# Kernel tuning notes

Hardware: AMD Instinct MI355X
Metric: run time of the kernel (lower is better)

## Reference

```python
import jax, jax.numpy as jnp
import numpy as np

B, E, K, U = 2048, 96, 8, 1024  # batch, word_emb_size, num_basis, num_units


def setup_inputs() -> dict:
    key = jax.random.key(0)
    k1, k2, k3, k4, k5 = jax.random.split(key, 5)
    inputs = jax.random.normal(k1, (B, E + K), dtype=jnp.float32)
    h_tm1 = jax.random.normal(k2, (B, U), dtype=jnp.float32)
    c_tm1 = jax.random.normal(k3, (B, U), dtype=jnp.float32)
    basis_kernel = jax.random.normal(k4, (E, K, 4 * U), dtype=jnp.float32) * 0.05
    basis_recurrent_kernel = jax.random.normal(k5, (U, K, 4 * U), dtype=jnp.float32) * 0.05
    bias = jnp.zeros((4 * U,), dtype=jnp.float32)
    return {
        "inputs": inputs,
        "h_tm1": h_tm1,
        "c_tm1": c_tm1,
        "basis_kernel": basis_kernel,
        "basis_recurrent_kernel": basis_recurrent_kernel,
        "bias": bias,
    }


def reference(inputs, h_tm1, c_tm1, basis_kernel, basis_recurrent_kernel, bias):
    word_emb_size = basis_kernel.shape[0]
    num_units = basis_recurrent_kernel.shape[0]
    x = inputs[:, :word_emb_size]           # [B, E]
    c_prob = inputs[:, word_emb_size:]      # [B, K]
    # Algebraically identical to composing a per-example kernel
    # (sum_k c_prob[b,k] * W[:,k,:]) and doing a per-example matmul:
    # z[b,z] = sum_e sum_k x[b,e] * c_prob[b,k] * W[e,k,z] (+ recurrent term).
    z = (jnp.einsum('be,ekz,bk->bz', x, basis_kernel, c_prob)
         + jnp.einsum('bu,ukz,bk->bz', h_tm1, basis_recurrent_kernel, c_prob)
         + bias)
    z0, z1, z2, z3 = jnp.split(z, 4, axis=1)  # each [B, U]
    i = jax.nn.sigmoid(z0)
    f = jax.nn.sigmoid(z1)
    c = f * c_tm1 + i * jnp.tanh(z2)
    o = jax.nn.sigmoid(z3)
    h = o * jnp.tanh(c)
    return (h, c)
```

## Files before the change

kernel.cpp:

```cpp
#include <hip/hip_runtime.h>
#include <stdint.h>
#include <stddef.h>

#define B_SZ   2048
#define E_SZ   96
#define K_SZ   8
#define U_SZ   1024
#define EK     (E_SZ * K_SZ)
#define KD     ((E_SZ + U_SZ) * K_SZ)
#define NZ     (4 * U_SZ)

typedef _Float16 f16_t;
typedef _Float16 f16x8 __attribute__((ext_vector_type(8)));
typedef float    f32x4 __attribute__((ext_vector_type(4)));

typedef __attribute__((address_space(3))) void       lds_void;
typedef const __attribute__((address_space(1))) void gbl_void;

__device__ __forceinline__ void gload16(const void* g, void* l) {
    __builtin_amdgcn_global_load_lds((gbl_void*)g, (lds_void*)l, 16, 0, 0);
}

__global__ __launch_bounds__(256) void build_a_kernel(
    const float* __restrict__ inputs,
    const float* __restrict__ h_tm1,
    f16_t* __restrict__ Ah)
{
    unsigned tid = blockIdx.x * 256u + threadIdx.x;
    unsigned b   = tid / 1120u;
    unsigned i8  = tid - b * 1120u;

    const float* row = inputs + (size_t)b * (E_SZ + K_SZ);
    f32x4 cp0 = *(const f32x4*)(row + E_SZ);
    f32x4 cp1 = *(const f32x4*)(row + E_SZ + 4);
    float cp[8] = {cp0[0], cp0[1], cp0[2], cp0[3], cp1[0], cp1[1], cp1[2], cp1[3]};

    float base = (i8 < (unsigned)E_SZ) ? row[i8]
                                       : h_tm1[(size_t)b * U_SZ + (i8 - E_SZ)];
    f16x8 hi;
    #pragma unroll
    for (int k = 0; k < 8; ++k)
        hi[k] = (f16_t)(base * cp[k]);
    *(f16x8*)(Ah + (size_t)b * KD + (size_t)i8 * 8) = hi;
}

__global__ __launch_bounds__(256) void transpose_w_kernel(
    const float* __restrict__ bk,
    const float* __restrict__ brk,
    f16_t* __restrict__ Wth)
{
    __shared__ float tile[64][65];
    int r0 = blockIdx.x * 64;
    int z0 = blockIdx.y * 64;
    const float* src = (r0 < EK) ? (bk + (size_t)r0 * NZ)
                                 : (brk + (size_t)(r0 - EK) * NZ);
    int t  = threadIdx.x;
    int rl = t >> 4;
    int c4 = (t & 15) * 4;

    #pragma unroll
    for (int i = 0; i < 4; ++i) {
        int r = rl + i * 16;
        f32x4 v = *(const f32x4*)(src + (size_t)r * NZ + z0 + c4);
        tile[r][c4 + 0] = v[0];
        tile[r][c4 + 1] = v[1];
        tile[r][c4 + 2] = v[2];
        tile[r][c4 + 3] = v[3];
    }
    __syncthreads();
    int zl = t >> 3;
    int c8 = (t & 7) * 8;
    #pragma unroll
    for (int i = 0; i < 2; ++i) {
        int z = zl + i * 32;
        f16x8 hi;
        #pragma unroll
        for (int j = 0; j < 8; ++j)
            hi[j] = (f16_t)tile[c8 + j][z];
        *(f16x8*)(Wth + (size_t)(z0 + z) * KD + r0 + c8) = hi;
    }
}

#define BM 256
#define BN 128
#define BK 64
#define NT 140
#define ABYTES (BM * BK * 2)
#define WBYTES (BN * BK * 2)
#define BUFB   (ABYTES + WBYTES)

__global__ __launch_bounds__(512, 2) void basis_lstm_gemm_kernel(
    const f16_t* __restrict__ Ah, const f16_t* __restrict__ Wth,
    const float* __restrict__ bias, const float* __restrict__ c_tm1,
    float* __restrict__ out)
{
    extern __shared__ __align__(16) char smem[];

    int id  = blockIdx.x;
    int v   = (id & 7) * 32 + (id >> 3);
    int bm0 = (v & 7) * BM;
    int jb0 = (v >> 3) * 32;

    int t    = threadIdx.x;
    int lane = t & 63;
    int w    = t >> 6;
    int wm   = w >> 1;
    int wn   = w & 1;
    int fr   = lane & 15;
    int hi4  = lane >> 4;

    f32x4 acc[4][4];
    #pragma unroll
    for (int m = 0; m < 4; ++m)
        #pragma unroll
        for (int n = 0; n < 4; ++n)
            acc[m][n] = (f32x4){0.f, 0.f, 0.f, 0.f};

    auto stage_part = [&](int buf, int kt, int part) {
        char* base = smem + buf * BUFB;
        int   ko   = kt * BK;
        #pragma unroll
        for (int i = 0; i < 2; ++i) {
            int q   = (part * 2 + i) * 512 + t;
            int row = q >> 3;
            int cc  = q & 7;
            size_t off = (size_t)(bm0 + row) * KD + ko + ((cc ^ (row & 7)) << 3);
            gload16(Ah + off, base + q * 16);
        }
        {
            int q  = part * 512 + t;
            int c  = q >> 3;
            int cc = q & 7;
            int z  = (((c >> 4) & 3) << 10) + jb0 + ((c >> 6) << 4) + (c & 15);
            size_t off = (size_t)z * KD + ko + ((cc ^ (c & 7)) << 3);
            gload16(Wth + off, base + ABYTES + q * 16);
        }
    };

    auto phase = [&](int buf, int kk, int kt2, bool do_stage) {
        const char* base = smem + buf * BUFB;
        f16x8 af[4], wf[4];
        #pragma unroll
        for (int m = 0; m < 4; ++m) {
            int ra = wm * 64 + m * 16 + fr;
            af[m] = *(const f16x8*)(base + ra * 128 + (((kk * 4 + hi4) ^ (ra & 7)) << 4));
        }
        #pragma unroll
        for (int n = 0; n < 4; ++n) {
            int rc = wn * 64 + n * 16 + fr;
            wf[n] = *(const f16x8*)(base + ABYTES + rc * 128 + (((kk * 4 + hi4) ^ (rc & 7)) << 4));
        }
        if (do_stage) stage_part((kt2 % 3), kt2, kk);
        __builtin_amdgcn_s_barrier();
        asm volatile("s_waitcnt lgkmcnt(0)" ::: "memory");
        __builtin_amdgcn_s_setprio(1);
        #pragma unroll
        for (int m = 0; m < 4; ++m)
            #pragma unroll
            for (int n = 0; n < 4; ++n)
                acc[m][n] = __builtin_amdgcn_mfma_f32_16x16x32_f16(af[m], wf[n], acc[m][n], 0, 0, 0);
        __builtin_amdgcn_s_setprio(0);
    };

    stage_part(0, 0, 0); stage_part(0, 0, 1);
    stage_part(1, 1, 0); stage_part(1, 1, 1);
    asm volatile("s_waitcnt vmcnt(6)" ::: "memory");
    __builtin_amdgcn_s_barrier();

    for (int kt = 0; kt < NT; ++kt) {
        bool st = (kt + 2 < NT);
        phase(kt % 3, 0, kt + 2, st);
        __builtin_amdgcn_s_barrier();
        phase(kt % 3, 1, kt + 2, st);
        if (st) {
            asm volatile("s_waitcnt vmcnt(6)" ::: "memory");
        } else {
            asm volatile("s_waitcnt vmcnt(0)" ::: "memory");
        }
        __builtin_amdgcn_s_barrier();
    }

    float* out_h = out;
    float* out_c = out + (size_t)B_SZ * U_SZ;
    int   jg = jb0 + wn * 16 + fr;
    float b0 = bias[jg];
    float b1 = bias[U_SZ + jg];
    float b2 = bias[2 * U_SZ + jg];
    float b3 = bias[3 * U_SZ + jg];
    #pragma unroll
    for (int m = 0; m < 4; ++m) {
        #pragma unroll
        for (int q = 0; q < 4; ++q) {
            int   br = bm0 + wm * 64 + m * 16 + hi4 * 4 + q;
            float zi = acc[m][0][q] + b0;
            float zf = acc[m][1][q] + b1;
            float zc = acc[m][2][q] + b2;
            float zo = acc[m][3][q] + b3;
            float ig = 1.f / (1.f + __expf(-zi));
            float fg = 1.f / (1.f + __expf(-zf));
            float og = 1.f / (1.f + __expf(-zo));
            float cn = fg * c_tm1[(size_t)br * U_SZ + jg] + ig * tanhf(zc);
            float hn = og * tanhf(cn);
            out_h[(size_t)br * U_SZ + jg] = hn;
            out_c[(size_t)br * U_SZ + jg] = cn;
        }
    }
}

extern "C" void kernel_launch(void* const* d_in, const int* in_sizes, int n_in,
                              void* d_out, int out_size, void* d_ws, size_t ws_size,
                              hipStream_t stream) {
    const float* inputs = (const float*)d_in[0];
    const float* h_tm1  = (const float*)d_in[1];
    const float* c_tm1  = (const float*)d_in[2];
    const float* bk     = (const float*)d_in[3];
    const float* brk    = (const float*)d_in[4];
    const float* bias   = (const float*)d_in[5];

    char*  ws  = (char*)d_ws;
    f16_t* Ah  = (f16_t*)(ws);
    f16_t* Wth = (f16_t*)(ws + 36700160u);

    hipFuncSetAttribute((const void*)basis_lstm_gemm_kernel,
                        hipFuncAttributeMaxDynamicSharedMemorySize, 3 * BUFB);

    hipLaunchKernelGGL(build_a_kernel, dim3(8960), dim3(256), 0, stream,
                       inputs, h_tm1, Ah);
    hipLaunchKernelGGL(transpose_w_kernel, dim3(140, 64), dim3(256), 0, stream,
                       bk, brk, Wth);
    hipLaunchKernelGGL(basis_lstm_gemm_kernel, dim3(256), dim3(512), 3 * BUFB, stream,
                       Ah, Wth, bias, c_tm1, (float*)d_out);
}
```

Measured before the change: 401.0 us.

## Switch GEMM to 32x32x16 MFMA with 4-stage BK=32 pipeline and LDS epilogue

Replaces the 16x16x32 MFMA tiling with 32x32x16 MFMA tiles (2x2 per wave) and halves BK to 32, moving from a 3-buffer to a 4-buffer LDS pipeline with a new XOR swizzle and split A/B staging across the two k-substeps. The epilogue now stages the accumulators through LDS so each thread processes the four gates for one column across 16 rows. The intent is fewer LDS fragment reads per FLOP and deeper prefetch to hide global latency. In exchange there are twice as many barriers per unit of K, the explicit lgkmcnt wait before the MFMAs is removed, and extra LDS traffic in the epilogue.

```diff
diff --git a/kernel.cpp b/kernel.cpp
--- a/kernel.cpp
+++ b/kernel.cpp
@@ -12,7 +12,8 @@
 
 typedef _Float16 f16_t;
 typedef _Float16 f16x8 __attribute__((ext_vector_type(8)));
-typedef float    f32x4 __attribute__((ext_vector_type(4)));
+typedef float    f32x4  __attribute__((ext_vector_type(4)));
+typedef float    f32x16 __attribute__((ext_vector_type(16)));
 
 typedef __attribute__((address_space(3))) void       lds_void;
 typedef const __attribute__((address_space(1))) void gbl_void;
@@ -83,11 +84,12 @@
 
 #define BM 256
 #define BN 128
-#define BK 64
-#define NT 140
-#define ABYTES (BM * BK * 2)
-#define WBYTES (BN * BK * 2)
-#define BUFB   (ABYTES + WBYTES)
+#define BK 32
+#define NT 280
+#define ABY (BM * BK * 2)
+#define WBY (BN * BK * 2)
+#define BUFB (ABY + WBY)
+#define SMEM_BYTES 131072
 
 __global__ __launch_bounds__(512, 2) void basis_lstm_gemm_kernel(
     const f16_t* __restrict__ Ah, const f16_t* __restrict__ Wth,
@@ -106,104 +108,127 @@
     int w    = t >> 6;
     int wm   = w >> 1;
     int wn   = w & 1;
-    int fr   = lane & 15;
-    int hi4  = lane >> 4;
-
-    f32x4 acc[4][4];
-    #pragma unroll
-    for (int m = 0; m < 4; ++m)
-        #pragma unroll
-        for (int n = 0; n < 4; ++n)
-            acc[m][n] = (f32x4){0.f, 0.f, 0.f, 0.f};
-
-    auto stage_part = [&](int buf, int kt, int part) {
-        char* base = smem + buf * BUFB;
-        int   ko   = kt * BK;
+    int l31  = lane & 31;
+    int lh   = lane >> 5;
+
+    f32x16 acc[2][2];
+    #pragma unroll
+    for (int mi = 0; mi < 2; ++mi)
+        #pragma unroll
+        for (int ni = 0; ni < 2; ++ni)
+            #pragma unroll
+            for (int e = 0; e < 16; ++e)
+                acc[mi][ni][e] = 0.f;
+
+    auto stageA = [&](int kt) {
+        char* buf = smem + (kt & 3) * BUFB;
+        int   ko  = kt * BK;
         #pragma unroll
         for (int i = 0; i < 2; ++i) {
-            int q   = (part * 2 + i) * 512 + t;
-            int row = q >> 3;
-            int cc  = q & 7;
-            size_t off = (size_t)(bm0 + row) * KD + ko + ((cc ^ (row & 7)) << 3);
-            gload16(Ah + off, base + q * 16);
-        }
-        {
-            int q  = part * 512 + t;
-            int c  = q >> 3;
-            int cc = q & 7;
-            int z  = (((c >> 4) & 3) << 10) + jb0 + ((c >> 6) << 4) + (c & 15);
-            size_t off = (size_t)z * KD + ko + ((cc ^ (c & 7)) << 3);
-            gload16(Wth + off, base + ABYTES + q * 16);
+            int q = i * 512 + t;
+            int row = q >> 2, cc = q & 3;
+            size_t off = (size_t)(bm0 + row) * KD + ko + ((cc ^ ((row ^ (row >> 2)) & 3)) << 3);
+            gload16(Ah + off, buf + q * 16);
         }
     };
-
-    auto phase = [&](int buf, int kk, int kt2, bool do_stage) {
-        const char* base = smem + buf * BUFB;
-        f16x8 af[4], wf[4];
-        #pragma unroll
-        for (int m = 0; m < 4; ++m) {
-            int ra = wm * 64 + m * 16 + fr;
-            af[m] = *(const f16x8*)(base + ra * 128 + (((kk * 4 + hi4) ^ (ra & 7)) << 4));
+    auto stageB = [&](int kt) {
+        char* buf = smem + (kt & 3) * BUFB + ABY;
+        int   ko  = kt * BK;
+        int q = t, c = q >> 2, cc = q & 3;
+        int z = ((c >> 5) << 10) + jb0 + (c & 31);
+        size_t off = (size_t)z * KD + ko + ((cc ^ ((c ^ (c >> 2)) & 3)) << 3);
+        gload16(Wth + off, buf + q * 16);
+    };
+
+    auto phase = [&](int kt, int ks, int stg) {
+        const char* buf = smem + (kt & 3) * BUFB;
+        f16x8 af[2], wf[2];
+        #pragma unroll
+        for (int mi = 0; mi < 2; ++mi) {
+            int r  = wm * 64 + mi * 32 + l31;
+            int sc = (ks * 2 + lh) ^ ((r ^ (r >> 2)) & 3);
+            af[mi] = *(const f16x8*)(buf + r * 64 + sc * 16);
         }
         #pragma unroll
-        for (int n = 0; n < 4; ++n) {
-            int rc = wn * 64 + n * 16 + fr;
-            wf[n] = *(const f16x8*)(base + ABYTES + rc * 128 + (((kk * 4 + hi4) ^ (rc & 7)) << 4));
+        for (int ni = 0; ni < 2; ++ni) {
+            int r  = wn * 64 + ni * 32 + l31;
+            int sc = (ks * 2 + lh) ^ ((r ^ (r >> 2)) & 3);
+            wf[ni] = *(const f16x8*)(buf + ABY + r * 64 + sc * 16);
         }
-        if (do_stage) stage_part((kt2 % 3), kt2, kk);
+        if (stg == 1) stageA(kt + 3);
+        else if (stg == 2) stageB(kt + 3);
         __builtin_amdgcn_s_barrier();
-        asm volatile("s_waitcnt lgkmcnt(0)" ::: "memory");
         __builtin_amdgcn_s_setprio(1);
         #pragma unroll
-        for (int m = 0; m < 4; ++m)
+        for (int mi = 0; mi < 2; ++mi)
             #pragma unroll
-            for (int n = 0; n < 4; ++n)
-                acc[m][n] = __builtin_amdgcn_mfma_f32_16x16x32_f16(af[m], wf[n], acc[m][n], 0, 0, 0);
+            for (int ni = 0; ni < 2; ++ni)
+                acc[mi][ni] = __builtin_amdgcn_mfma_f32_32x32x16_f16(af[mi], wf[ni], acc[mi][ni], 0, 0, 0);
         __builtin_amdgcn_s_setprio(0);
     };
 
-    stage_part(0, 0, 0); stage_part(0, 0, 1);
-    stage_part(1, 1, 0); stage_part(1, 1, 1);
+    stageA(0); stageB(0);
+    stageA(1); stageB(1);
+    stageA(2); stageB(2);
     asm volatile("s_waitcnt vmcnt(6)" ::: "memory");
     __builtin_amdgcn_s_barrier();
 
-    for (int kt = 0; kt < NT; ++kt) {
-        bool st = (kt + 2 < NT);
-        phase(kt % 3, 0, kt + 2, st);
+    for (int kt = 0; kt < NT - 3; ++kt) {
+        phase(kt, 0, 1);
         __builtin_amdgcn_s_barrier();
-        phase(kt % 3, 1, kt + 2, st);
-        if (st) {
-            asm volatile("s_waitcnt vmcnt(6)" ::: "memory");
-        } else {
-            asm volatile("s_waitcnt vmcnt(0)" ::: "memory");
-        }
+        phase(kt, 1, 2);
+        asm volatile("s_waitcnt vmcnt(6)" ::: "memory");
         __builtin_amdgcn_s_barrier();
     }
-
-    float* out_h = out;
-    float* out_c = out + (size_t)B_SZ * U_SZ;
-    int   jg = jb0 + wn * 16 + fr;
+    phase(NT - 3, 0, 0); __builtin_amdgcn_s_barrier();
+    phase(NT - 3, 1, 0);
+    asm volatile("s_waitcnt vmcnt(3)" ::: "memory");
+    __builtin_amdgcn_s_barrier();
+    phase(NT - 2, 0, 0); __builtin_amdgcn_s_barrier();
+    phase(NT - 2, 1, 0);
+    asm volatile("s_waitcnt vmcnt(0)" ::: "memory");
+    __builtin_amdgcn_s_barrier();
+    phase(NT - 1, 0, 0); __builtin_amdgcn_s_barrier();
+    phase(NT - 1, 1, 0);
+    __syncthreads();
+
+    float* zb = (float*)smem;
+    #pragma unroll
+    for (int mi = 0; mi < 2; ++mi)
+        #pragma unroll
+        for (int ni = 0; ni < 2; ++ni)
+            #pragma unroll
+            for (int r = 0; r < 16; ++r) {
+                int row = wm * 64 + mi * 32 + (r & 3) + 8 * (r >> 2) + 4 * lh;
+                int col = wn * 64 + ni * 32 + l31;
+                zb[row * 128 + col] = acc[mi][ni][r];
+            }
+    __syncthreads();
+
+    int jj = t & 31;
+    int rg = t >> 5;
+    int jg = jb0 + jj;
     float b0 = bias[jg];
     float b1 = bias[U_SZ + jg];
     float b2 = bias[2 * U_SZ + jg];
     float b3 = bias[3 * U_SZ + jg];
-    #pragma unroll
-    for (int m = 0; m < 4; ++m) {
-        #pragma unroll
-        for (int q = 0; q < 4; ++q) {
-            int   br = bm0 + wm * 64 + m * 16 + hi4 * 4 + q;
-            float zi = acc[m][0][q] + b0;
-            float zf = acc[m][1][q] + b1;
-            float zc = acc[m][2][q] + b2;
-            float zo = acc[m][3][q] + b3;
-            float ig = 1.f / (1.f + __expf(-zi));
-            float fg = 1.f / (1.f + __expf(-zf));
-            float og = 1.f / (1.f + __expf(-zo));
-            float cn = fg * c_tm1[(size_t)br * U_SZ + jg] + ig * tanhf(zc);
-            float hn = og * tanhf(cn);
-            out_h[(size_t)br * U_SZ + jg] = hn;
-            out_c[(size_t)br * U_SZ + jg] = cn;
-        }
+    float* out_h = out;
+    float* out_c = out + (size_t)B_SZ * U_SZ;
+    #pragma unroll
+    for (int i = 0; i < 16; ++i) {
+        int   row = rg * 16 + i;
+        int   br  = bm0 + row;
+        float zi = zb[row * 128 +  0 + jj] + b0;
+        float zf = zb[row * 128 + 32 + jj] + b1;
+        float zc = zb[row * 128 + 64 + jj] + b2;
+        float zo = zb[row * 128 + 96 + jj] + b3;
+        float ig = 1.f / (1.f + __expf(-zi));
+        float fg = 1.f / (1.f + __expf(-zf));
+        float og = 1.f / (1.f + __expf(-zo));
+        float cn = fg * c_tm1[(size_t)br * U_SZ + jg] + ig * tanhf(zc);
+        float hn = og * tanhf(cn);
+        out_h[(size_t)br * U_SZ + jg] = hn;
+        out_c[(size_t)br * U_SZ + jg] = cn;
     }
 }
 
@@ -222,12 +247,12 @@
     f16_t* Wth = (f16_t*)(ws + 36700160u);
 
     hipFuncSetAttribute((const void*)basis_lstm_gemm_kernel,
-                        hipFuncAttributeMaxDynamicSharedMemorySize, 3 * BUFB);
+                        hipFuncAttributeMaxDynamicSharedMemorySize, SMEM_BYTES);
 
     hipLaunchKernelGGL(build_a_kernel, dim3(8960), dim3(256), 0, stream,
                        inputs, h_tm1, Ah);
     hipLaunchKernelGGL(transpose_w_kernel, dim3(140, 64), dim3(256), 0, stream,
                        bk, brk, Wth);
-    hipLaunchKernelGGL(basis_lstm_gemm_kernel, dim3(256), dim3(512), 3 * BUFB, stream,
+    hipLaunchKernelGGL(basis_lstm_gemm_kernel, dim3(256), dim3(512), SMEM_BYTES, stream,
                        Ah, Wth, bias, c_tm1, (float*)d_out);
 }
```

After: 421.8 us. 1.05x slower.
